# Kernel optimization log

Measured on AMD Instinct MI355X. Metric: run time of the kernel, lower is better.

The kernel has to match this reference:

```python
import jax, jax.numpy as jnp
import numpy as np

HIDDEN = 1024
HEADS = 16
HEAD_DIM = HIDDEN // HEADS


def setup_inputs() -> dict:
    key = jax.random.key(0)
    ks = jax.random.split(key, 5)
    x = jax.random.normal(ks[0], (4, 2048, HIDDEN), dtype=jnp.float32)
    s = 1.0 / np.sqrt(HIDDEN)
    W_qkv = jax.random.normal(ks[1], (HIDDEN, 3 * HIDDEN), dtype=jnp.float32) * s
    b_qkv = jax.random.normal(ks[2], (3 * HIDDEN,), dtype=jnp.float32) * s
    W_out = jax.random.normal(ks[3], (HIDDEN, HIDDEN), dtype=jnp.float32) * s
    b_out = jax.random.normal(ks[4], (HIDDEN,), dtype=jnp.float32) * s
    return {"x": x, "W_qkv": W_qkv, "b_qkv": b_qkv, "W_out": W_out, "b_out": b_out}


def reference(x, W_qkv, b_qkv, W_out, b_out):
    B, S, _ = x.shape
    qkv = x @ W_qkv + b_qkv                       # [B,S,3H]
    qkv = qkv.reshape(B, S, 3, HEADS, HEAD_DIM)
    q, k, v = jnp.moveaxis(qkv, 2, 0)             # each [B,S,nh,hd]
    scale = 1.0 / np.sqrt(HEAD_DIM)
    scores = jnp.einsum('bqhd,bkhd->bhqk', q, k) * scale
    probs = jax.nn.softmax(scores, axis=-1)       # dropout p=0 (eval): identity
    attn = jnp.einsum('bhqk,bkhd->bqhd', probs, v)
    attn = attn.reshape(B, S, HIDDEN)
    return attn @ W_out + b_out
```

## Files before the change

kernel.cpp:

```cpp
#include <hip/hip_runtime.h>

#define SEQ    2048
#define BATCH  4
#define HID    1024
#define NH     16
#define MTOT   (BATCH * SEQ)

typedef __attribute__((ext_vector_type(8)))  short          short8;
typedef __attribute__((ext_vector_type(4)))  float          f32x4;
typedef __attribute__((ext_vector_type(16))) float          f32x16;
typedef __attribute__((ext_vector_type(8)))  unsigned short ushort8v;
typedef __attribute__((ext_vector_type(4)))  unsigned int   uint4v;

#define QSCL 0.125f

__device__ __forceinline__ float bf2f(unsigned short u) {
    return __uint_as_float(((unsigned int)u) << 16);
}
__device__ __forceinline__ unsigned short f2bf(float f) {
    unsigned int u = __float_as_uint(f);
    u += 0x7fffu + ((u >> 16) & 1u);
    return (unsigned short)(u >> 16);
}
__device__ __forceinline__ unsigned int pk2bf(float lo, float hi) {
    unsigned int ul = __float_as_uint(lo) + 0x8000u;
    unsigned int uh = __float_as_uint(hi) + 0x8000u;
    return __builtin_amdgcn_perm(uh, ul, 0x07060302u);
}

__device__ __forceinline__ void gl_lds16(const void* g, void* l) {
    __builtin_amdgcn_global_load_lds(
        (__attribute__((address_space(1))) void*)g,
        (__attribute__((address_space(3))) void*)l, 16, 0, 0);
}

__device__ __forceinline__ int swz64(int row, int col) {
    return row * 64 + ((((col >> 3) ^ (row & 7))) << 3) + (col & 7);
}

__device__ __forceinline__ int gidx64(int row, int kq) {
    return (row * 8 + ((kq + (row & 7)) & 7)) * 8;
}

__global__ __launch_bounds__(256)
void cvt_x(const float* __restrict__ x, unsigned short* __restrict__ xb)
{
    const size_t i = ((size_t)blockIdx.x * 256 + threadIdx.x) * 4;
    const float4 f = *(const float4*)(x + i);
    uint2 u;
    u.x = pk2bf(f.x, f.y);
    u.y = pk2bf(f.z, f.w);
    *(uint2*)(xb + i) = u;
}

__global__ __launch_bounds__(256)
void transpose_cvt(const float* __restrict__ W, unsigned short* __restrict__ Wt,
                   int K, int N)
{
    __shared__ unsigned short T[32][33];
    const int n0 = blockIdx.x * 32, k0 = blockIdx.y * 32;
    const int tr = threadIdx.x >> 3, tc = (threadIdx.x & 7) * 4;
    const float4 f = *(const float4*)(W + (size_t)(k0 + tr) * N + n0 + tc);
    T[tr][tc + 0] = f2bf(f.x);
    T[tr][tc + 1] = f2bf(f.y);
    T[tr][tc + 2] = f2bf(f.z);
    T[tr][tc + 3] = f2bf(f.w);
    __syncthreads();
    ushort4 u;
    u.x = T[tc + 0][tr]; u.y = T[tc + 1][tr];
    u.z = T[tc + 2][tr]; u.w = T[tc + 3][tr];
    *(ushort4*)(Wt + (size_t)(n0 + tr) * K + k0 + tc) = u;
}

template<bool OUTF32, bool VSPLIT, bool BIASROW>
__global__ __launch_bounds__(256)
void gemm_mfma(const unsigned short* __restrict__ A,
               const unsigned short* __restrict__ Bt,
               const float* __restrict__ bias, void* __restrict__ Cptr,
               int lda, int ldc, int K)
{
    __shared__ unsigned short As[128 * 64];
    __shared__ unsigned short Bs[128 * 64];

    const int tid = threadIdx.x;
    const int wave = tid >> 6, lane = tid & 63;
    const int quad = lane >> 4, lm = lane & 15;
    const int wm = wave & 1, wn = wave >> 1;
    const int m0 = blockIdx.y * 128, n0 = blockIdx.x * 128;

    const unsigned short* aSrc[4];
    const unsigned short* bSrc[4];
    unsigned short* aDst[4];
    unsigned short* bDst[4];
    #pragma unroll
    for (int j = 0; j < 4; ++j) {
        const int g = (wave * 4 + j) * 64 + lane;
        const int row = g >> 3;
        const int kq = ((g & 7) - (row & 7)) & 7;
        aSrc[j] = A  + (size_t)(m0 + row) * lda + kq * 8;
        bSrc[j] = Bt + (size_t)(n0 + row) * K   + kq * 8;
        aDst[j] = &As[g * 8];
        bDst[j] = &Bs[g * 8];
    }

    f32x4 acc[4][4];
    #pragma unroll
    for (int i = 0; i < 4; ++i)
        #pragma unroll
        for (int j = 0; j < 4; ++j)
            acc[i][j] = (f32x4){0.f, 0.f, 0.f, 0.f};

    int aOff[2][4], bOff[2][4];
    #pragma unroll
    for (int h = 0; h < 2; ++h)
        #pragma unroll
        for (int i = 0; i < 4; ++i) {
            aOff[h][i] = gidx64(wm * 64 + i * 16 + lm, h * 4 + quad);
            bOff[h][i] = gidx64(wn * 64 + i * 16 + lm, h * 4 + quad);
        }

    for (int k0 = 0; k0 < K; k0 += 64) {
        __syncthreads();
        #pragma unroll
        for (int j = 0; j < 4; ++j) gl_lds16(aSrc[j] + k0, aDst[j]);
        #pragma unroll
        for (int j = 0; j < 4; ++j) gl_lds16(bSrc[j] + k0, bDst[j]);
        __syncthreads();

        #pragma unroll
        for (int h = 0; h < 2; ++h) {
            short8 af[4], bf[4];
            #pragma unroll
            for (int i = 0; i < 4; ++i) af[i] = *(const short8*)&As[aOff[h][i]];
            #pragma unroll
            for (int j = 0; j < 4; ++j) bf[j] = *(const short8*)&Bs[bOff[h][j]];
            #pragma unroll
            for (int i = 0; i < 4; ++i)
                #pragma unroll
                for (int j = 0; j < 4; ++j)
                    acc[i][j] = __builtin_amdgcn_mfma_f32_16x16x32_bf16(
                        af[i], bf[j], acc[i][j], 0, 0, 0);
        }
    }

    float bj[4];
    float br[4][4];
    if constexpr (BIASROW) {
        #pragma unroll
        for (int i = 0; i < 4; ++i) {
            const float4 t =
                *(const float4*)(bias + m0 + wm * 64 + i * 16 + quad * 4);
            br[i][0] = t.x; br[i][1] = t.y; br[i][2] = t.z; br[i][3] = t.w;
        }
    } else {
        #pragma unroll
        for (int j = 0; j < 4; ++j) bj[j] = bias[n0 + wn * 64 + j * 16 + lm];
    }

    #pragma unroll
    for (int i = 0; i < 4; ++i) {
        #pragma unroll
        for (int j = 0; j < 4; ++j) {
            const int col = n0 + wn * 64 + j * 16 + lm;
            #pragma unroll
            for (int rr = 0; rr < 4; ++rr) {
                const int row = m0 + wm * 64 + i * 16 + quad * 4 + rr;
                float v = acc[i][j][rr] + (BIASROW ? br[i][rr] : bj[j]);
                if constexpr (VSPLIT) {
                    if (col < 1024) v *= QSCL;
                    ((unsigned short*)Cptr)[(size_t)row * ldc + col] = f2bf(v);
                } else if constexpr (OUTF32) {
                    ((float*)Cptr)[(size_t)row * ldc + col] = v;
                } else {
                    ((unsigned short*)Cptr)[(size_t)row * ldc + col] = f2bf(v);
                }
            }
        }
    }
}

__global__ __launch_bounds__(256, 2)
void attn_mfma(unsigned short* __restrict__ qk,
               const unsigned short* __restrict__ Vt)
{
    const int qt = blockIdx.x, hh = blockIdx.y, b = blockIdx.z;
    const size_t row0 = (size_t)b * SEQ;
    const int tid = threadIdx.x;
    const int wave = tid >> 6, lane = tid & 63;
    const int l5 = lane >> 5, lm = lane & 31;

    __shared__ unsigned short Ks[64 * 64];
    __shared__ unsigned short Vst[64 * 64];

    const int qbase = qt * 256 + wave * 64;

    short8 qf[2][4];
    #pragma unroll
    for (int qg = 0; qg < 2; ++qg)
        #pragma unroll
        for (int ks = 0; ks < 4; ++ks)
            qf[qg][ks] = *(const short8*)(
                qk + (row0 + qbase + qg * 32 + lm) * 2048 + hh * 64 + ks * 16 + l5 * 8);

    f32x16 oacc[2][2];
    #pragma unroll
    for (int dg = 0; dg < 2; ++dg)
        #pragma unroll
        for (int qg = 0; qg < 2; ++qg)
            #pragma unroll
            for (int e = 0; e < 16; ++e) oacc[dg][qg][e] = 0.f;
    float lrun[2] = {0.f, 0.f};

    const int srow = tid >> 2;
    const int scol = (tid & 3) * 16;

    const unsigned short* kbase = qk + 1024 + hh * 64;
    const unsigned short* vbase =
        Vt + (size_t)(hh * 64 + srow) * (size_t)MTOT + (size_t)b * SEQ;

    ushort8v kp0, kp1, vp0, vp1;
    {
        const unsigned short* kp = kbase + (row0 + srow) * 2048 + scol;
        kp0 = *(const ushort8v*)kp;  kp1 = *(const ushort8v*)(kp + 8);
        vp0 = *(const ushort8v*)(vbase + scol);
        vp1 = *(const ushort8v*)(vbase + scol + 8);
    }

    for (int kt = 0; kt < SEQ; kt += 64) {
        __syncthreads();
        *(ushort8v*)&Ks[swz64(srow, scol)]      = kp0;
        *(ushort8v*)&Ks[swz64(srow, scol + 8)]  = kp1;
        *(ushort8v*)&Vst[swz64(srow, scol)]     = vp0;
        *(ushort8v*)&Vst[swz64(srow, scol + 8)] = vp1;
        __syncthreads();

        {
            const int nk = (kt + 64 < SEQ) ? kt + 64 : kt;
            const unsigned short* kp = kbase + (row0 + nk + srow) * 2048 + scol;
            kp0 = *(const ushort8v*)kp;  kp1 = *(const ushort8v*)(kp + 8);
            vp0 = *(const ushort8v*)(vbase + nk + scol);
            vp1 = *(const ushort8v*)(vbase + nk + scol + 8);
        }

        #pragma unroll
        for (int kg = 0; kg < 2; ++kg) {
            short8 aK[4];
            #pragma unroll
            for (int ks = 0; ks < 4; ++ks)
                aK[ks] = *(const short8*)&Ks[swz64(kg * 32 + lm, ks * 16 + l5 * 8)];

            f32x16 s[2];
            #pragma unroll
            for (int qg = 0; qg < 2; ++qg) {
                #pragma unroll
                for (int e = 0; e < 16; ++e) s[qg][e] = 0.f;
                #pragma unroll
                for (int ks = 0; ks < 4; ++ks)
                    s[qg] = __builtin_amdgcn_mfma_f32_32x32x16_bf16(
                        aK[ks], qf[qg][ks], s[qg], 0, 0, 0);
                float ls = 0.f;
                #pragma unroll
                for (int rg = 0; rg < 4; ++rg) {
                    const float p0 = __expf(s[qg][rg * 4 + 0]);
                    const float p1 = __expf(s[qg][rg * 4 + 1]);
                    const float p2 = __expf(s[qg][rg * 4 + 2]);
                    const float p3 = __expf(s[qg][rg * 4 + 3]);
                    s[qg][rg * 4 + 0] = p0; s[qg][rg * 4 + 1] = p1;
                    s[qg][rg * 4 + 2] = p2; s[qg][rg * 4 + 3] = p3;
                    ls += (p0 + p1) + (p2 + p3);
                }
                lrun[qg] += ls;
            }

            #pragma unroll
            for (int step = 0; step < 2; ++step) {
                const int ks = kg * 2 + step;
                const short8 aV0 =
                    *(const short8*)&Vst[swz64(lm,      ks * 16 + l5 * 8)];
                const short8 aV1 =
                    *(const short8*)&Vst[swz64(32 + lm, ks * 16 + l5 * 8)];
                #pragma unroll
                for (int qg = 0; qg < 2; ++qg) {
                    const int b0 = step * 8;
                    const unsigned int u  = pk2bf(s[qg][b0 + 0], s[qg][b0 + 1]);
                    const unsigned int vv = pk2bf(s[qg][b0 + 2], s[qg][b0 + 3]);
                    const unsigned int u2 = pk2bf(s[qg][b0 + 4], s[qg][b0 + 5]);
                    const unsigned int v2 = pk2bf(s[qg][b0 + 6], s[qg][b0 + 7]);
                    const auto rA =
                        __builtin_amdgcn_permlane32_swap(u,  u2, false, false);
                    const auto rB =
                        __builtin_amdgcn_permlane32_swap(vv, v2, false, false);
                    uint4v wv;
                    wv.x = rA[0]; wv.y = rB[0]; wv.z = rA[1]; wv.w = rB[1];
                    const short8 bP = __builtin_bit_cast(short8, wv);
                    oacc[0][qg] = __builtin_amdgcn_mfma_f32_32x32x16_bf16(
                        aV0, bP, oacc[0][qg], 0, 0, 0);
                    oacc[1][qg] = __builtin_amdgcn_mfma_f32_32x32x16_bf16(
                        aV1, bP, oacc[1][qg], 0, 0, 0);
                }
            }
        }
    }

    float linv[2];
    #pragma unroll
    for (int qg = 0; qg < 2; ++qg) {
        const float lt = lrun[qg] + __shfl_xor(lrun[qg], 32);
        linv[qg] = 1.f / lt;
    }

    #pragma unroll
    for (int dg = 0; dg < 2; ++dg)
        #pragma unroll
        for (int qg = 0; qg < 2; ++qg) {
            unsigned short* orow =
                qk + (row0 + qbase + qg * 32 + lm) * 2048 + hh * 64;
            #pragma unroll
            for (int rg = 0; rg < 4; ++rg) {
                const int d0 = dg * 32 + rg * 8 + l5 * 4;
                ushort4 st;
                st.x = f2bf(oacc[dg][qg][rg * 4 + 0] * linv[qg]);
                st.y = f2bf(oacc[dg][qg][rg * 4 + 1] * linv[qg]);
                st.z = f2bf(oacc[dg][qg][rg * 4 + 2] * linv[qg]);
                st.w = f2bf(oacc[dg][qg][rg * 4 + 3] * linv[qg]);
                *(ushort4*)(orow + d0) = st;
            }
        }
}

__global__ __launch_bounds__(256)
void qproj(const float* __restrict__ A, const float* __restrict__ W,
           const float* __restrict__ bias, unsigned short* __restrict__ outus)
{
    __shared__ float As[64][17];
    __shared__ float Bs[16][64];
    const int tid = threadIdx.x;
    const int tx = tid & 15, ty = tid >> 4;
    const int m0 = blockIdx.y * 64, n0 = blockIdx.x * 64;
    const int ar = tid >> 2, ac = (tid & 3) * 4;
    const int br = tid >> 4, bc = (tid & 15) * 4;
    float acc[4][4] = {{0.f}};
    for (int k0 = 0; k0 < HID; k0 += 16) {
        const float4 av = *(const float4*)(A + (size_t)(m0 + ar) * HID + k0 + ac);
        As[ar][ac + 0] = av.x; As[ar][ac + 1] = av.y;
        As[ar][ac + 2] = av.z; As[ar][ac + 3] = av.w;
        *(float4*)&Bs[br][bc] =
            *(const float4*)(W + (size_t)(k0 + br) * 3072 + n0 + bc);
        __syncthreads();
        #pragma unroll
        for (int kk = 0; kk < 16; ++kk) {
            float a[4];
            #pragma unroll
            for (int i = 0; i < 4; ++i) a[i] = As[ty * 4 + i][kk];
            const float4 b4 = *(const float4*)&Bs[kk][tx * 4];
            const float bv[4] = {b4.x, b4.y, b4.z, b4.w};
            #pragma unroll
            for (int i = 0; i < 4; ++i)
                #pragma unroll
                for (int j = 0; j < 4; ++j)
                    acc[i][j] = fmaf(a[i], bv[j], acc[i][j]);
        }
        __syncthreads();
    }
    float bb[4];
    #pragma unroll
    for (int j = 0; j < 4; ++j) bb[j] = bias[n0 + tx * 4 + j];
    #pragma unroll
    for (int i = 0; i < 4; ++i) {
        ushort4 st;
        st.x = f2bf(acc[i][0] + bb[0]); st.y = f2bf(acc[i][1] + bb[1]);
        st.z = f2bf(acc[i][2] + bb[2]); st.w = f2bf(acc[i][3] + bb[3]);
        *(ushort4*)(outus + (size_t)(m0 + ty * 4 + i) * 2048 + 1024 + n0 + tx * 4) = st;
    }
}

__global__ __launch_bounds__(256)
void kv_inplace(const float* __restrict__ W, const float* __restrict__ bias,
                unsigned short* __restrict__ xu)
{
    const float* xf = (const float*)xu;
    __shared__ unsigned short Asb[16][1032];
    __shared__ float Bs[16][68];
    const int tid = threadIdx.x;
    const int m0 = blockIdx.x * 16;
    const int tx = tid & 15, ty = tid >> 4;
    #pragma unroll 4
    for (int i = 0; i < 16; ++i) {
        const float4 v = *(const float4*)(xf + (size_t)(m0 + i) * HID + tid * 4);
        ushort4 s;
        s.x = f2bf(v.x); s.y = f2bf(v.y); s.z = f2bf(v.z); s.w = f2bf(v.w);
        *(ushort4*)&Asb[i][tid * 4] = s;
    }
    __syncthreads();
    for (int n0 = 0; n0 < 2048; n0 += 64) {
        float acc[4] = {0.f, 0.f, 0.f, 0.f};
        for (int k0 = 0; k0 < HID; k0 += 16) {
            *(float4*)&Bs[ty][tx * 4] =
                *(const float4*)(W + (size_t)(k0 + ty) * 3072 + 1024 + n0 + tx * 4);
            __syncthreads();
            #pragma unroll
            for (int kk = 0; kk < 16; ++kk) {
                const float a = bf2f(Asb[ty][k0 + kk]);
                const float4 b4 = *(const float4*)&Bs[kk][tx * 4];
                acc[0] = fmaf(a, b4.x, acc[0]); acc[1] = fmaf(a, b4.y, acc[1]);
                acc[2] = fmaf(a, b4.z, acc[2]); acc[3] = fmaf(a, b4.w, acc[3]);
            }
            __syncthreads();
        }
        const int n = n0 + tx * 4;
        ushort4 s;
        s.x = f2bf(acc[0] + bias[1024 + n + 0]);
        s.y = f2bf(acc[1] + bias[1024 + n + 1]);
        s.z = f2bf(acc[2] + bias[1024 + n + 2]);
        s.w = f2bf(acc[3] + bias[1024 + n + 3]);
        *(ushort4*)(xu + (size_t)(m0 + ty) * 2048 + n) = s;
    }
}

__global__ __launch_bounds__(256)
void attn_fwd(const unsigned short* __restrict__ xu,
              unsigned short* __restrict__ outus)
{
    const int qt = blockIdx.x, h = blockIdx.y, b = blockIdx.z;
    const int s0 = qt * 16;
    const size_t row0 = (size_t)b * SEQ;
    const int tid = threadIdx.x;
    const int qi = tid >> 4, tj = tid & 15;
    __shared__ float Ksh[64][68];
    __shared__ float Vsh[64][68];
    __shared__ float Psh[16][68];
    float qreg[64];
    {
        const uint4* qp =
            (const uint4*)(outus + (row0 + s0 + qi) * 2048 + 1024 + h * 64);
        #pragma unroll
        for (int i = 0; i < 8; ++i) {
            uint4 u = qp[i];
            const unsigned int w[4] = {u.x, u.y, u.z, u.w};
            #pragma unroll
            for (int j = 0; j < 4; ++j) {
                qreg[i * 8 + j * 2 + 0] = __uint_as_float(w[j] << 16) * 0.125f;
                qreg[i * 8 + j * 2 + 1] = __uint_as_float(w[j] & 0xffff0000u) * 0.125f;
            }
        }
    }
    float mrun = -1e30f, lrunv = 0.f;
    float oacc[4] = {0.f, 0.f, 0.f, 0.f};
    const int lr = tid >> 3, lc = (tid & 7) * 8;
    for (int kt = 0; kt < SEQ; kt += 64) {
        __syncthreads();
        #pragma unroll
        for (int half = 0; half < 2; ++half) {
            const int r = lr + half * 32;
            const size_t rowoff = (row0 + kt + r) * 2048 + h * 64 + lc;
            uint4 ku = *(const uint4*)(xu + rowoff);
            uint4 vu = *(const uint4*)(xu + rowoff + 1024);
            float4 f0, f1;
            f0.x = __uint_as_float(ku.x << 16); f0.y = __uint_as_float(ku.x & 0xffff0000u);
            f0.z = __uint_as_float(ku.y << 16); f0.w = __uint_as_float(ku.y & 0xffff0000u);
            f1.x = __uint_as_float(ku.z << 16); f1.y = __uint_as_float(ku.z & 0xffff0000u);
            f1.z = __uint_as_float(ku.w << 16); f1.w = __uint_as_float(ku.w & 0xffff0000u);
            *(float4*)&Ksh[r][lc]     = f0;
            *(float4*)&Ksh[r][lc + 4] = f1;
            f0.x = __uint_as_float(vu.x << 16); f0.y = __uint_as_float(vu.x & 0xffff0000u);
            f0.z = __uint_as_float(vu.y << 16); f0.w = __uint_as_float(vu.y & 0xffff0000u);
            f1.x = __uint_as_float(vu.z << 16); f1.y = __uint_as_float(vu.z & 0xffff0000u);
            f1.z = __uint_as_float(vu.w << 16); f1.w = __uint_as_float(vu.w & 0xffff0000u);
            *(float4*)&Vsh[r][lc]     = f0;
            *(float4*)&Vsh[r][lc + 4] = f1;
        }
        __syncthreads();
        float sc[4];
        #pragma unroll
        for (int u = 0; u < 4; ++u) {
            const int kk = tj + 16 * u;
            float s = 0.f;
            #pragma unroll
            for (int d = 0; d < 64; ++d) s = fmaf(qreg[d], Ksh[kk][d], s);
            sc[u] = s;
        }
        float tmax = fmaxf(fmaxf(sc[0], sc[1]), fmaxf(sc[2], sc[3]));
        #pragma unroll
        for (int off = 8; off >= 1; off >>= 1)
            tmax = fmaxf(tmax, __shfl_xor(tmax, off, 16));
        const float mnew = fmaxf(mrun, tmax);
        const float alpha = __expf(mrun - mnew);
        float psum = 0.f;
        #pragma unroll
        for (int u = 0; u < 4; ++u) {
            const float p = __expf(sc[u] - mnew);
            Psh[qi][tj + 16 * u] = p;
            psum += p;
        }
        #pragma unroll
        for (int off = 8; off >= 1; off >>= 1)
            psum += __shfl_xor(psum, off, 16);
        lrunv = lrunv * alpha + psum;
        mrun = mnew;
        oacc[0] *= alpha; oacc[1] *= alpha; oacc[2] *= alpha; oacc[3] *= alpha;
        __syncthreads();
        #pragma unroll 8
        for (int kk = 0; kk < 64; ++kk) {
            const float p = Psh[qi][kk];
            const float4 v4 = *(const float4*)&Vsh[kk][tj * 4];
            oacc[0] = fmaf(p, v4.x, oacc[0]); oacc[1] = fmaf(p, v4.y, oacc[1]);
            oacc[2] = fmaf(p, v4.z, oacc[2]); oacc[3] = fmaf(p, v4.w, oacc[3]);
        }
    }
    const float inv = 1.f / lrunv;
    ushort4 st;
    st.x = f2bf(oacc[0] * inv); st.y = f2bf(oacc[1] * inv);
    st.z = f2bf(oacc[2] * inv); st.w = f2bf(oacc[3] * inv);
    *(ushort4*)(outus + (row0 + s0 + qi) * 2048 + h * 64 + tj * 4) = st;
}

__global__ __launch_bounds__(256)
void out_final(const float* __restrict__ W, const float* __restrict__ bias,
               unsigned short* __restrict__ outus)
{
    float* outf = (float*)outus;
    __shared__ unsigned short Asb[16][1032];
    __shared__ float Bs[16][68];
    const int tid = threadIdx.x;
    const int m0 = blockIdx.x * 16;
    const int tx = tid & 15, ty = tid >> 4;
    #pragma unroll 4
    for (int i = 0; i < 16; ++i)
        *(ushort4*)&Asb[i][tid * 4] =
            *(const ushort4*)(outus + (size_t)(m0 + i) * 2048 + tid * 4);
    __syncthreads();
    for (int n0 = 0; n0 < 1024; n0 += 64) {
        float acc[4] = {0.f, 0.f, 0.f, 0.f};
        for (int k0 = 0; k0 < HID; k0 += 16) {
            *(float4*)&Bs[ty][tx * 4] =
                *(const float4*)(W + (size_t)(k0 + ty) * HID + n0 + tx * 4);
            __syncthreads();
            #pragma unroll
            for (int kk = 0; kk < 16; ++kk) {
                const float a = bf2f(Asb[ty][k0 + kk]);
                const float4 b4 = *(const float4*)&Bs[kk][tx * 4];
                acc[0] = fmaf(a, b4.x, acc[0]); acc[1] = fmaf(a, b4.y, acc[1]);
                acc[2] = fmaf(a, b4.z, acc[2]); acc[3] = fmaf(a, b4.w, acc[3]);
            }
            __syncthreads();
        }
        const int n = n0 + tx * 4;
        float4 st;
        st.x = acc[0] + bias[n + 0]; st.y = acc[1] + bias[n + 1];
        st.z = acc[2] + bias[n + 2]; st.w = acc[3] + bias[n + 3];
        *(float4*)(outf + (size_t)(m0 + ty) * HID + n) = st;
    }
}

extern "C" void kernel_launch(void* const* d_in, const int* in_sizes, int n_in,
                              void* d_out, int out_size, void* d_ws, size_t ws_size,
                              hipStream_t stream) {
    const float* x     = (const float*)d_in[0];
    const float* W_qkv = (const float*)d_in[1];
    const float* b_qkv = (const float*)d_in[2];
    const float* W_out = (const float*)d_in[3];
    const float* b_out = (const float*)d_in[4];

    dim3 blk(256);

    if (ws_size >= (size_t)56 * 1024 * 1024) {
        unsigned short* qkbuf  = (unsigned short*)d_ws;
        unsigned short* vtbuf  = qkbuf + (size_t)MTOT * 2048;
        unsigned short* wqkv_t = vtbuf + (size_t)1024 * MTOT;
        unsigned short* wout_t = wqkv_t + (size_t)3072 * 1024;
        unsigned short* xb     = (unsigned short*)d_out;

        cvt_x<<<dim3(MTOT * HID / 1024), blk, 0, stream>>>(x, xb);
        transpose_cvt<<<dim3(3072 / 32, 1024 / 32), blk, 0, stream>>>(
            W_qkv, wqkv_t, 1024, 3072);
        transpose_cvt<<<dim3(1024 / 32, 1024 / 32), blk, 0, stream>>>(
            W_out, wout_t, 1024, 1024);
        gemm_mfma<false, true, false><<<dim3(2048 / 128, MTOT / 128), blk, 0, stream>>>(
            xb, wqkv_t, b_qkv, (void*)qkbuf, 1024, 2048, 1024);
        gemm_mfma<false, false, true><<<dim3(MTOT / 128, 1024 / 128), blk, 0, stream>>>(
            wqkv_t + (size_t)2048 * 1024, xb, b_qkv + 2048, (void*)vtbuf,
            1024, MTOT, 1024);
        attn_mfma<<<dim3(SEQ / 256, NH, BATCH), blk, 0, stream>>>(qkbuf, vtbuf);
        gemm_mfma<true, false, false><<<dim3(1024 / 128, MTOT / 128), blk, 0, stream>>>(
            qkbuf, wout_t, b_out, d_out, 2048, 1024, 1024);
    } else {
        unsigned short* outus = (unsigned short*)d_out;
        unsigned short* xu    = (unsigned short*)d_in[0];
        qproj<<<dim3(HID / 64, MTOT / 64), blk, 0, stream>>>(x, W_qkv, b_qkv, outus);
        kv_inplace<<<dim3(MTOT / 16), blk, 0, stream>>>(W_qkv, b_qkv, xu);
        attn_fwd<<<dim3(SEQ / 16, NH, BATCH), blk, 0, stream>>>(xu, outus);
        out_final<<<dim3(MTOT / 16), blk, 0, stream>>>(W_out, b_out, outus);
    }
}
```

Measured before the change: 290.3 us.

## Double-buffer K/V tiles with direct global-to-LDS loads in attention kernel

```diff
diff --git a/kernel.cpp b/kernel.cpp
--- a/kernel.cpp
+++ b/kernel.cpp
@@ -189,8 +189,8 @@
     const int wave = tid >> 6, lane = tid & 63;
     const int l5 = lane >> 5, lm = lane & 31;
 
-    __shared__ unsigned short Ks[64 * 64];
-    __shared__ unsigned short Vst[64 * 64];
+    __shared__ unsigned short Ks[2][64 * 64];
+    __shared__ unsigned short Vs[2][64 * 64];
 
     const int qbase = qt * 256 + wave * 64;
 
@@ -211,53 +211,59 @@
             for (int e = 0; e < 16; ++e) oacc[dg][qg][e] = 0.f;
     float lrun[2] = {0.f, 0.f};
 
-    const int srow = tid >> 2;
-    const int scol = (tid & 3) * 16;
-
-    const unsigned short* kbase = qk + 1024 + hh * 64;
-    const unsigned short* vbase =
-        Vt + (size_t)(hh * 64 + srow) * (size_t)MTOT + (size_t)b * SEQ;
-
-    ushort8v kp0, kp1, vp0, vp1;
-    {
-        const unsigned short* kp = kbase + (row0 + srow) * 2048 + scol;
-        kp0 = *(const ushort8v*)kp;  kp1 = *(const ushort8v*)(kp + 8);
-        vp0 = *(const ushort8v*)(vbase + scol);
-        vp1 = *(const ushort8v*)(vbase + scol + 8);
-    }
-
+    const unsigned short* kSrc[2];
+    const unsigned short* vSrc[2];
+    int dOff[2];
+    #pragma unroll
+    for (int jj = 0; jj < 2; ++jj) {
+        const int g = (wave * 2 + jj) * 64 + lane;
+        const int row = g >> 3, slot = g & 7;
+        const int colg = slot ^ (row & 7);
+        kSrc[jj] = qk + 1024 + hh * 64 + (row0 + row) * 2048 + colg * 8;
+        vSrc[jj] = Vt + (size_t)(hh * 64 + row) * (size_t)MTOT
+                      + (size_t)b * SEQ + colg * 8;
+        dOff[jj] = g * 8;
+    }
+
+    #pragma unroll
+    for (int jj = 0; jj < 2; ++jj) {
+        gl_lds16(kSrc[jj], &Ks[0][dOff[jj]]);
+        gl_lds16(vSrc[jj], &Vs[0][dOff[jj]]);
+    }
+    __syncthreads();
+
+    int cur = 0;
     for (int kt = 0; kt < SEQ; kt += 64) {
-        __syncthreads();
-        *(ushort8v*)&Ks[swz64(srow, scol)]      = kp0;
-        *(ushort8v*)&Ks[swz64(srow, scol + 8)]  = kp1;
-        *(ushort8v*)&Vst[swz64(srow, scol)]     = vp0;
-        *(ushort8v*)&Vst[swz64(srow, scol + 8)] = vp1;
-        __syncthreads();
-
-        {
-            const int nk = (kt + 64 < SEQ) ? kt + 64 : kt;
-            const unsigned short* kp = kbase + (row0 + nk + srow) * 2048 + scol;
-            kp0 = *(const ushort8v*)kp;  kp1 = *(const ushort8v*)(kp + 8);
-            vp0 = *(const ushort8v*)(vbase + nk + scol);
-            vp1 = *(const ushort8v*)(vbase + nk + scol + 8);
-        }
+        if (kt + 64 < SEQ) {
+            const size_t ko = (size_t)(kt + 64) * 2048;
+            const int vo = kt + 64;
+            #pragma unroll
+            for (int jj = 0; jj < 2; ++jj) {
+                gl_lds16(kSrc[jj] + ko, &Ks[cur ^ 1][dOff[jj]]);
+                gl_lds16(vSrc[jj] + vo, &Vs[cur ^ 1][dOff[jj]]);
+            }
+        }
+        const unsigned short* ksc = Ks[cur];
+        const unsigned short* vsc = Vs[cur];
 
         #pragma unroll
         for (int kg = 0; kg < 2; ++kg) {
             short8 aK[4];
             #pragma unroll
             for (int ks = 0; ks < 4; ++ks)
-                aK[ks] = *(const short8*)&Ks[swz64(kg * 32 + lm, ks * 16 + l5 * 8)];
+                aK[ks] = *(const short8*)&ksc[swz64(kg * 32 + lm, ks * 16 + l5 * 8)];
 
             f32x16 s[2];
             #pragma unroll
             for (int qg = 0; qg < 2; ++qg) {
                 #pragma unroll
                 for (int e = 0; e < 16; ++e) s[qg][e] = 0.f;
+                __builtin_amdgcn_s_setprio(1);
                 #pragma unroll
                 for (int ks = 0; ks < 4; ++ks)
                     s[qg] = __builtin_amdgcn_mfma_f32_32x32x16_bf16(
                         aK[ks], qf[qg][ks], s[qg], 0, 0, 0);
+                __builtin_amdgcn_s_setprio(0);
                 float ls = 0.f;
                 #pragma unroll
                 for (int rg = 0; rg < 4; ++rg) {
@@ -276,9 +282,9 @@
             for (int step = 0; step < 2; ++step) {
                 const int ks = kg * 2 + step;
                 const short8 aV0 =
-                    *(const short8*)&Vst[swz64(lm,      ks * 16 + l5 * 8)];
+                    *(const short8*)&vsc[swz64(lm,      ks * 16 + l5 * 8)];
                 const short8 aV1 =
-                    *(const short8*)&Vst[swz64(32 + lm, ks * 16 + l5 * 8)];
+                    *(const short8*)&vsc[swz64(32 + lm, ks * 16 + l5 * 8)];
                 #pragma unroll
                 for (int qg = 0; qg < 2; ++qg) {
                     const int b0 = step * 8;
@@ -293,13 +299,17 @@
                     uint4v wv;
                     wv.x = rA[0]; wv.y = rB[0]; wv.z = rA[1]; wv.w = rB[1];
                     const short8 bP = __builtin_bit_cast(short8, wv);
+                    __builtin_amdgcn_s_setprio(1);
                     oacc[0][qg] = __builtin_amdgcn_mfma_f32_32x32x16_bf16(
                         aV0, bP, oacc[0][qg], 0, 0, 0);
                     oacc[1][qg] = __builtin_amdgcn_mfma_f32_32x32x16_bf16(
                         aV1, bP, oacc[1][qg], 0, 0, 0);
+                    __builtin_amdgcn_s_setprio(0);
                 }
             }
         }
+        __syncthreads();
+        cur ^= 1;
     }
 
     float linv[2];
```

After: 286.4 us. Within noise of the previous version (-1.3%).
